# Performance work log

Hardware: AMD Instinct MI355X
Metric: run time of the kernel (lower is better)

## Reference

```python
import math
import jax, jax.numpy as jnp
import numpy as np

B, H, W, CV = 8, 64, 64, 256
T, CT = 77, 512
NH, TOP_M = 8, 5
CLAMP = 2.0

def _ln(x, g, b, eps=1e-5):
    mu = x.mean(-1, keepdims=True)
    var = ((x - mu) ** 2).mean(-1, keepdims=True)
    return (x - mu) / jnp.sqrt(var + eps) * g + b

def _l2norm(x, eps=1e-6):
    n = jnp.sqrt((x * x).sum(-1, keepdims=True))
    return x / jnp.maximum(n, eps)

def _xavier(key, fan_in, fan_out):
    a = math.sqrt(6.0 / (fan_in + fan_out))
    return jax.random.uniform(key, (fan_in, fan_out), jnp.float32, -a, a)

def setup_inputs() -> dict:
    key = jax.random.key(0)
    ks = jax.random.split(key, 12)
    inp = {
        'visual_features': jax.random.normal(ks[0], (B, H, W, CV), jnp.float32),
        'text_features': jax.random.normal(ks[1], (B, T, CT), jnp.float32),
        'Wq': _xavier(ks[2], CV, CV), 'bq': jnp.zeros((CV,), jnp.float32),
        'Wk': _xavier(ks[3], CT, CV), 'bk': jnp.zeros((CV,), jnp.float32),
        'Wv': _xavier(ks[4], CT, CV), 'bv': jnp.zeros((CV,), jnp.float32),
        'Wo': _xavier(ks[5], CV, CV), 'bo': jnp.zeros((CV,), jnp.float32),
        'g1': jnp.ones((CV,), jnp.float32), 'b1': jnp.zeros((CV,), jnp.float32),
        'g2': jnp.ones((CV,), jnp.float32), 'b2': jnp.zeros((CV,), jnp.float32),
        'W_ffn1': jax.random.normal(ks[6], (CV, 4 * CV), jnp.float32) * 0.02,
        'b_ffn1': jnp.zeros((4 * CV,), jnp.float32),
        'W_ffn2': jax.random.normal(ks[7], (4 * CV, CV), jnp.float32) * 0.02,
        'b_ffn2': jnp.zeros((CV,), jnp.float32),
        'logit_scale': jnp.float32(math.log(1.0 / 0.07)),
        'alpha': jnp.float32(0.1),
    }
    return inp

def _topm_mask(sim, m):
    # keep only top-m entries along last axis (scatter of top-k indices)
    t = sim.shape[-1]
    _, topi = jax.lax.top_k(sim, m)
    keep = jax.vmap(lambda idx: jnp.zeros((t,), bool).at[idx].set(True))(
        topi.reshape(-1, m)).reshape(sim.shape)
    return jnp.where(keep, sim, -jnp.inf)

def _forward(visual_features, text_features, Wq, bq, Wk, bk, Wv, bv, Wo, bo,
             g1, b1, g2, b2, W_ffn1, b_ffn1, W_ffn2, b_ffn2, logit_scale, alpha):
    b, h, w, cv = visual_features.shape
    n = h * w
    dh = cv // NH
    x = _ln(visual_features, g1, b1).reshape(b, n, cv)      # Pre-LN, (B,N,Cv)
    q = (x @ Wq + bq).reshape(b, n, NH, dh)
    k = (text_features @ Wk + bk).reshape(b, T, NH, dh)
    v = (text_features @ Wv + bv).reshape(b, T, NH, dh)
    q = _l2norm(q); k = _l2norm(k)                           # cosine attention
    scale = jnp.exp(jnp.clip(logit_scale, -CLAMP, CLAMP)) / jnp.sqrt(jnp.float32(dh))
    sim = jnp.einsum('bnhd,bthd->bnht', q, k) * scale        # (B,N,H,T)
    pad = jnp.abs(text_features).sum(-1) <= 1e-6             # (B,T) pad tokens
    sim = jnp.where(pad[:, None, None, :], -jnp.inf, sim)
    sim = _topm_mask(sim, TOP_M)
    attn = jax.nn.softmax(sim, axis=-1)
    all_pad = pad.all(axis=1)                                # (B,)
    attn = jnp.where(all_pad[:, None, None, None], 0.0, attn)
    aligned = jnp.einsum('bnht,bthd->bnhd', attn, v).reshape(b, n, cv)
    aligned = aligned @ Wo + bo
    y = x + alpha * aligned
    y = _ln(y, g2, b2)
    hdn = jax.nn.gelu(y @ W_ffn1 + b_ffn1, approximate=False)
    y = y + (hdn @ W_ffn2 + b_ffn2)
    return y.reshape(b, h, w, cv)

def reference(visual_features, text_features, Wq, bq, Wk, bk, Wv, bv, Wo, bo,
              g1, b1, g2, b2, W_ffn1, b_ffn1, W_ffn2, b_ffn2, logit_scale, alpha):
    return _forward(visual_features, text_features, Wq, bq, Wk, bk, Wv, bv, Wo, bo,
                    g1, b1, g2, b2, W_ffn1, b_ffn1, W_ffn2, b_ffn2, logit_scale, alpha)
```

## Files before the change

kernel.cpp:

```cpp
#include <hip/hip_runtime.h>
#include <math.h>

#define NB   8
#define NPIX 4096
#define MROW 32768
#define CV_  256
#define TT   77
#define CT_  512
#define NH_  8
#define DH_  32
#define BT_  616

typedef __bf16 bf16x8 __attribute__((ext_vector_type(8)));
typedef float  f32x4  __attribute__((ext_vector_type(4)));

__device__ __forceinline__ float bf2f(unsigned short u) {
  return __uint_as_float(((unsigned)u) << 16);
}
__device__ __forceinline__ unsigned short f2b(float f) {
  unsigned u = __float_as_uint(f);
  return (unsigned short)((u + 0x7FFFu + ((u >> 16) & 1u)) >> 16);
}
__device__ __forceinline__ unsigned pack2(float lo, float hi) {
  return ((unsigned)f2b(hi) << 16) | (unsigned)f2b(lo);
}
__device__ __forceinline__ void async_copy16(const unsigned short* g,
                                             unsigned short* l) {
  __builtin_amdgcn_global_load_lds(
      (const __attribute__((address_space(1))) void*)g,
      (__attribute__((address_space(3))) void*)l, 16, 0, 0);
}
__device__ __forceinline__ float gelu_t(float v) {
  float p = v * fmaf(0.0713548162726f, v * v, 1.59576912161f);
  float e = __expf(p);
  return v - v / (e + 1.0f);
}

__global__ __launch_bounds__(256) void prep_kernel(
    const float* __restrict__ visual, const float* __restrict__ g1,
    const float* __restrict__ b1, unsigned short* __restrict__ xbuf,
    const float* __restrict__ s0, const float* __restrict__ s1,
    const float* __restrict__ s2, const float* __restrict__ s3,
    const float* __restrict__ s4, const float* __restrict__ s5,
    unsigned short* __restrict__ d0, unsigned short* __restrict__ d1,
    unsigned short* __restrict__ d2, unsigned short* __restrict__ d3,
    unsigned short* __restrict__ d4, unsigned short* __restrict__ d5,
    const float* __restrict__ bk, const float* __restrict__ bv,
    float* __restrict__ bkv, const float* __restrict__ text,
    float* __restrict__ padb) {
  __shared__ unsigned short tl[64 * 68];
  int bx = blockIdx.x;
  int tid = threadIdx.x;
  int wave = tid >> 6, lane = tid & 63;
  if (bx < 8192) {
    int row = bx * 4 + wave;
    size_t base = (size_t)row * 256 + lane * 4;
    float4 f = *reinterpret_cast<const float4*>(visual + base);
    float v0 = f.x, v1 = f.y, v2 = f.z, v3 = f.w;
    float s = v0 + v1 + v2 + v3;
    float q = v0 * v0 + v1 * v1 + v2 * v2 + v3 * v3;
#pragma unroll
    for (int off = 1; off < 64; off <<= 1) {
      s += __shfl_xor(s, off);
      q += __shfl_xor(q, off);
    }
    float mean = s * (1.0f / 256.0f);
    float var  = q * (1.0f / 256.0f) - mean * mean;
    float rstd = rsqrtf(var + 1e-5f);
    float4 gv = *reinterpret_cast<const float4*>(g1 + lane * 4);
    float4 bv4 = *reinterpret_cast<const float4*>(b1 + lane * 4);
    ushort4 o;
    o.x = f2b((v0 - mean) * rstd * gv.x + bv4.x);
    o.y = f2b((v1 - mean) * rstd * gv.y + bv4.y);
    o.z = f2b((v2 - mean) * rstd * gv.z + bv4.z);
    o.w = f2b((v3 - mean) * rstd * gv.w + bv4.w);
    *reinterpret_cast<ushort4*>(xbuf + base) = o;
    return;
  }
  if (bx < 8416) {
    int ti = bx - 8192;
    const float* src; unsigned short* dst; int R, C, m;
    if      (ti < 16)  { src = s0; dst = d0; R = 256;  C = 256;  m = ti; }
    else if (ti < 48)  { src = s1; dst = d1; R = 512;  C = 256;  m = ti - 16; }
    else if (ti < 80)  { src = s2; dst = d2; R = 512;  C = 256;  m = ti - 48; }
    else if (ti < 96)  { src = s3; dst = d3; R = 256;  C = 256;  m = ti - 80; }
    else if (ti < 160) { src = s4; dst = d4; R = 256;  C = 1024; m = ti - 96; }
    else               { src = s5; dst = d5; R = 1024; C = 256;  m = ti - 160; }
    int tpc = C >> 6;
    int tr = m / tpc, tc = m % tpc;
#pragma unroll
    for (int i = 0; i < 4; ++i) {
      int lin = tid + i * 256;
      int r = lin >> 4, c4 = (lin & 15) * 4;
      float4 f = *reinterpret_cast<const float4*>(
          src + (size_t)(tr * 64 + r) * C + tc * 64 + c4);
      tl[(c4 + 0) * 68 + r] = f2b(f.x);
      tl[(c4 + 1) * 68 + r] = f2b(f.y);
      tl[(c4 + 2) * 68 + r] = f2b(f.z);
      tl[(c4 + 3) * 68 + r] = f2b(f.w);
    }
    __syncthreads();
#pragma unroll
    for (int i = 0; i < 4; ++i) {
      int lin = tid + i * 256;
      int c = lin >> 4, r4 = (lin & 15) * 4;
      ushort4 u = *reinterpret_cast<const ushort4*>(&tl[c * 68 + r4]);
      *reinterpret_cast<ushort4*>(
          dst + (size_t)(tc * 64 + c) * R + tr * 64 + r4) = u;
    }
    return;
  }
  if (bx == 8416) {
    bkv[tid] = bk[tid];
    bkv[256 + tid] = bv[tid];
    return;
  }
  {
    int row = (bx - 8417) * 4 + wave;
    const float* tr = text + (size_t)row * CT_ + lane * 8;
    float4 f0 = *reinterpret_cast<const float4*>(tr);
    float4 f1 = *reinterpret_cast<const float4*>(tr + 4);
    float s = fabsf(f0.x) + fabsf(f0.y) + fabsf(f0.z) + fabsf(f0.w)
            + fabsf(f1.x) + fabsf(f1.y) + fabsf(f1.z) + fabsf(f1.w);
#pragma unroll
    for (int off = 1; off < 64; off <<= 1) s += __shfl_xor(s, off);
    if (lane == 0) padb[row] = (s <= 1e-6f) ? 1.0f : 0.0f;
  }
}

__global__ __launch_bounds__(256) void qkv_kernel(
    const unsigned short* __restrict__ xb, const unsigned short* __restrict__ WqT,
    const float* __restrict__ bq, unsigned short* __restrict__ qout,
    const float* __restrict__ text, const unsigned short* __restrict__ WkvT,
    const float* __restrict__ bkv, float* __restrict__ kout,
    float* __restrict__ vout) {
  __shared__ unsigned short lA[4096];
  __shared__ unsigned short lB[4096];
  int tid = threadIdx.x;
  int lane = tid & 63, wave = tid >> 6;
  int l15 = lane & 15, quad = lane >> 4;
  if (blockIdx.x < 512) {
    int bm = (blockIdx.x >> 1) * 128, bn = (blockIdx.x & 1) * 128;
    int wm = (wave & 1) * 64, wn = (wave >> 1) * 64;
    int crow = lane >> 2, ccol = (lane & 3) * 8;
    f32x4 acc[4][4] = {};
    for (int k0 = 0; k0 < 256; k0 += 32) {
#pragma unroll
      for (int ch = 0; ch < 2; ++ch) {
        int c = wave * 2 + ch;
        async_copy16(xb + (size_t)(bm + c * 16 + crow) * 256 + k0 + ccol,
                     &lA[c * 512]);
        async_copy16(WqT + (size_t)(bn + c * 16 + crow) * 256 + k0 + ccol,
                     &lB[c * 512]);
      }
      __syncthreads();
      bf16x8 af[4], bfr[4];
#pragma unroll
      for (int mi = 0; mi < 4; ++mi)
        af[mi] = *reinterpret_cast<const bf16x8*>(&lA[(wm + mi * 16 + l15) * 32 + quad * 8]);
#pragma unroll
      for (int ni = 0; ni < 4; ++ni)
        bfr[ni] = *reinterpret_cast<const bf16x8*>(&lB[(wn + ni * 16 + l15) * 32 + quad * 8]);
#pragma unroll
      for (int mi = 0; mi < 4; ++mi)
#pragma unroll
        for (int ni = 0; ni < 4; ++ni)
          acc[mi][ni] = __builtin_amdgcn_mfma_f32_16x16x32_bf16(af[mi], bfr[ni],
                                                                acc[mi][ni], 0, 0, 0);
      __syncthreads();
    }
#pragma unroll
    for (int mi = 0; mi < 4; ++mi) {
#pragma unroll
      for (int ni = 0; ni < 4; ++ni) {
        int gcol = bn + wn + ni * 16 + l15;
        float bsf = bq[gcol];
#pragma unroll
        for (int r = 0; r < 4; ++r) {
          int grow = bm + wm + mi * 16 + quad * 4 + r;
          qout[(size_t)grow * 256 + gcol] = f2b(acc[mi][ni][r] + bsf);
        }
      }
    }
  } else {
    int i = blockIdx.x - 512;
    int bm = (i % 10) * 64, bn = (i / 10) * 64;
    int srow = tid >> 2, sc8 = (tid & 3) * 8;
    int wm = (wave & 1) * 32, wn = (wave >> 1) * 32;
    f32x4 acc[2][2] = {};
    int gm = bm + srow, gn = bn + srow;
    const bool aok = (gm < BT_);
    for (int k0 = 0; k0 < CT_; k0 += 32) {
      uint4 apk = make_uint4(0, 0, 0, 0);
      if (aok) {
        const float* Af = text + (size_t)gm * CT_ + k0 + sc8;
        float4 f0 = *reinterpret_cast<const float4*>(Af);
        float4 f1 = *reinterpret_cast<const float4*>(Af + 4);
        apk.x = pack2(f0.x, f0.y); apk.y = pack2(f0.z, f0.w);
        apk.z = pack2(f1.x, f1.y); apk.w = pack2(f1.z, f1.w);
      }
      uint4 bpk = *reinterpret_cast<const uint4*>(WkvT + (size_t)gn * CT_ + k0 + sc8);
      *reinterpret_cast<uint4*>(&lA[srow * 40 + sc8]) = apk;
      *reinterpret_cast<uint4*>(&lB[srow * 40 + sc8]) = bpk;
      __syncthreads();
      bf16x8 a0 = *reinterpret_cast<const bf16x8*>(&lA[(wm + l15) * 40 + quad * 8]);
      bf16x8 a1 = *reinterpret_cast<const bf16x8*>(&lA[(wm + 16 + l15) * 40 + quad * 8]);
      bf16x8 b0 = *reinterpret_cast<const bf16x8*>(&lB[(wn + l15) * 40 + quad * 8]);
      bf16x8 b1 = *reinterpret_cast<const bf16x8*>(&lB[(wn + 16 + l15) * 40 + quad * 8]);
      acc[0][0] = __builtin_amdgcn_mfma_f32_16x16x32_bf16(a0, b0, acc[0][0], 0, 0, 0);
      acc[0][1] = __builtin_amdgcn_mfma_f32_16x16x32_bf16(a0, b1, acc[0][1], 0, 0, 0);
      acc[1][0] = __builtin_amdgcn_mfma_f32_16x16x32_bf16(a1, b0, acc[1][0], 0, 0, 0);
      acc[1][1] = __builtin_amdgcn_mfma_f32_16x16x32_bf16(a1, b1, acc[1][1], 0, 0, 0);
      __syncthreads();
    }
#pragma unroll
    for (int mt = 0; mt < 2; ++mt) {
#pragma unroll
      for (int nt = 0; nt < 2; ++nt) {
        int gcol = bn + wn + nt * 16 + l15;
        float bsf = bkv[gcol];
#pragma unroll
        for (int r = 0; r < 4; ++r) {
          int grow = bm + wm + mt * 16 + quad * 4 + r;
          if (grow >= BT_) continue;
          float v = acc[mt][nt][r] + bsf;
          if (gcol < 256) kout[(size_t)grow * 256 + gcol] = v;
          else            vout[(size_t)grow * 256 + gcol - 256] = v;
        }
      }
    }
  }
}

__global__ __launch_bounds__(256) void gemm_oln(
    const unsigned short* __restrict__ A, const unsigned short* __restrict__ Bt,
    const float* __restrict__ bias, const unsigned short* __restrict__ xres,
    const float* __restrict__ alpha_ptr,
    const float* __restrict__ g2, const float* __restrict__ b2,
    unsigned short* __restrict__ ybf, float* __restrict__ yf32) {
  __shared__ unsigned short sm[16384];
  unsigned short* lA = sm;
  unsigned short* lB = sm + 2048;
  unsigned short* yt = sm;
  const int K = 256;
  int tid = threadIdx.x;
  int bm = blockIdx.x * 64;
  int lane = tid & 63, wave = tid >> 6;
  int wm = (wave & 1) * 32, wn = (wave >> 1) * 128;
  int l15 = lane & 15, quad = lane >> 4;
  int crow = lane >> 2, ccol = (lane & 3) * 8;
  f32x4 acc[2][8] = {};
  for (int k0 = 0; k0 < K; k0 += 32) {
    async_copy16(A + (size_t)(bm + wave * 16 + crow) * K + k0 + ccol,
                 &lA[wave * 512]);
#pragma unroll
    for (int ch = wave; ch < 16; ch += 4)
      async_copy16(Bt + (size_t)(ch * 16 + crow) * K + k0 + ccol,
                   &lB[ch * 512]);
    __syncthreads();
    bf16x8 af[2], bfr[8];
#pragma unroll
    for (int mi = 0; mi < 2; ++mi)
      af[mi] = *reinterpret_cast<const bf16x8*>(&lA[(wm + mi * 16 + l15) * 32 + quad * 8]);
#pragma unroll
    for (int ni = 0; ni < 8; ++ni)
      bfr[ni] = *reinterpret_cast<const bf16x8*>(&lB[(wn + ni * 16 + l15) * 32 + quad * 8]);
#pragma unroll
    for (int mi = 0; mi < 2; ++mi)
#pragma unroll
      for (int ni = 0; ni < 8; ++ni)
        acc[mi][ni] = __builtin_amdgcn_mfma_f32_16x16x32_bf16(af[mi], bfr[ni],
                                                              acc[mi][ni], 0, 0, 0);
    __syncthreads();
  }
  float alpha = *alpha_ptr;
#pragma unroll
  for (int mi = 0; mi < 2; ++mi) {
#pragma unroll
    for (int ni = 0; ni < 8; ++ni) {
      int gcol = wn + ni * 16 + l15;
      float bsf = bias[gcol];
#pragma unroll
      for (int r = 0; r < 4; ++r) {
        int lrow = wm + mi * 16 + quad * 4 + r;
        float v = acc[mi][ni][r] + bsf;
        float y0 = bf2f(xres[(size_t)(bm + lrow) * 256 + gcol]) + alpha * v;
        yt[lrow * 256 + gcol] = f2b(y0);
      }
    }
  }
  __syncthreads();
  for (int it = 0; it < 16; ++it) {
    int row = wave * 16 + it;
    ushort4 u = *reinterpret_cast<const ushort4*>(&yt[row * 256 + lane * 4]);
    float v0 = bf2f(u.x), v1 = bf2f(u.y), v2 = bf2f(u.z), v3 = bf2f(u.w);
    float s = v0 + v1 + v2 + v3;
    float q = v0 * v0 + v1 * v1 + v2 * v2 + v3 * v3;
#pragma unroll
    for (int off = 1; off < 64; off <<= 1) {
      s += __shfl_xor(s, off);
      q += __shfl_xor(q, off);
    }
    float mean = s * (1.0f / 256.0f);
    float var  = q * (1.0f / 256.0f) - mean * mean;
    float rstd = rsqrtf(var + 1e-5f);
    float4 gv = *reinterpret_cast<const float4*>(g2 + lane * 4);
    float4 bv = *reinterpret_cast<const float4*>(b2 + lane * 4);
    float o0 = (v0 - mean) * rstd * gv.x + bv.x;
    float o1 = (v1 - mean) * rstd * gv.y + bv.y;
    float o2 = (v2 - mean) * rstd * gv.z + bv.z;
    float o3 = (v3 - mean) * rstd * gv.w + bv.w;
    size_t base = (size_t)(bm + row) * 256 + lane * 4;
    ushort4 ob;
    ob.x = f2b(o0); ob.y = f2b(o1); ob.z = f2b(o2); ob.w = f2b(o3);
    *reinterpret_cast<ushort4*>(ybf + base) = ob;
    *reinterpret_cast<float4*>(yf32 + base) = make_float4(o0, o1, o2, o3);
  }
}

#define SSTR 83
#define VSTR 33
#define NEGBIG -3.0e38f
__device__ __forceinline__ void ins5(float sv, float& tv0, float& tv1,
                                     float& tv2, float& tv3, float& tv4) {
  bool g0 = sv > tv0, g1 = sv > tv1, g2 = sv > tv2, g3 = sv > tv3, g4 = sv > tv4;
  tv4 = g4 ? (g3 ? tv3 : sv) : tv4;
  tv3 = g3 ? (g2 ? tv2 : sv) : tv3;
  tv2 = g2 ? (g1 ? tv1 : sv) : tv2;
  tv1 = g1 ? (g0 ? tv0 : sv) : tv1;
  tv0 = g0 ? sv : tv0;
}
__global__ __launch_bounds__(256) void attn_kernel(
    unsigned short* qa, const float* __restrict__ k,
    const float* __restrict__ v, const float* __restrict__ padb,
    const float* __restrict__ ls_ptr) {
  __shared__ unsigned short qb[64 * 40];
  __shared__ unsigned short kb[80 * 40];
  __shared__ float S[64 * SSTR];
  __shared__ float vs[TT * VSTR];
  __shared__ float rn[64];
  __shared__ float scs[80];
  __shared__ int allpad_s;
  int tid = threadIdx.x;
  int h = blockIdx.y, b = blockIdx.z;
  size_t qbase = ((size_t)b * NPIX + blockIdx.x * 64) * CV_ + h * DH_;
  size_t kvbase = (size_t)b * TT * CV_ + h * DH_;
  float ls = *ls_ptr;
  ls = fminf(fmaxf(ls, -2.0f), 2.0f);
  float scale = expf(ls) * 0.17677669529663687f;
  if (tid == 0) allpad_s = 1;
  __syncthreads();
  int qrow = tid >> 2, qq = tid & 3;
  uint4 qv4 = *reinterpret_cast<const uint4*>(qa + qbase + (size_t)qrow * CV_ + qq * 8);
  *reinterpret_cast<uint4*>(&qb[qrow * 40 + qq * 8]) = qv4;
  {
    float ssq = 0.f;
    unsigned w[4] = {qv4.x, qv4.y, qv4.z, qv4.w};
#pragma unroll
    for (int i = 0; i < 4; ++i) {
      float a = bf2f((unsigned short)(w[i] & 0xFFFF));
      float bb = bf2f((unsigned short)(w[i] >> 16));
      ssq += a * a + bb * bb;
    }
    ssq += __shfl_xor(ssq, 1);
    ssq += __shfl_xor(ssq, 2);
    if (qq == 0) rn[qrow] = scale / fmaxf(sqrtf(ssq), 1e-6f);
  }
  if (tid < 154) {
    int kr = tid >> 1, kh = tid & 1;
    const float* kp = k + kvbase + (size_t)kr * CV_ + kh * 16;
    float4 f0 = *reinterpret_cast<const float4*>(kp);
    float4 f1 = *reinterpret_cast<const float4*>(kp + 4);
    float4 f2 = *reinterpret_cast<const float4*>(kp + 8);
    float4 f3 = *reinterpret_cast<const float4*>(kp + 12);
    float ks2 = f0.x*f0.x + f0.y*f0.y + f0.z*f0.z + f0.w*f0.w
              + f1.x*f1.x + f1.y*f1.y + f1.z*f1.z + f1.w*f1.w
              + f2.x*f2.x + f2.y*f2.y + f2.z*f2.z + f2.w*f2.w
              + f3.x*f3.x + f3.y*f3.y + f3.z*f3.z + f3.w*f3.w;
    uint4 p0, p1;
    p0.x = pack2(f0.x, f0.y); p0.y = pack2(f0.z, f0.w);
    p0.z = pack2(f1.x, f1.y); p0.w = pack2(f1.z, f1.w);
    p1.x = pack2(f2.x, f2.y); p1.y = pack2(f2.z, f2.w);
    p1.z = pack2(f3.x, f3.y); p1.w = pack2(f3.z, f3.w);
    *reinterpret_cast<uint4*>(&kb[kr * 40 + kh * 16]) = p0;
    *reinterpret_cast<uint4*>(&kb[kr * 40 + kh * 16 + 8]) = p1;
    ks2 += __shfl_xor(ks2, 1);
    if (kh == 0) {
      float p = padb[b * TT + kr];
      float sc = (p == 0.0f) ? 1.0f / fmaxf(sqrtf(ks2), 1e-6f) : 0.0f;
      scs[kr] = sc;
      if (sc > 0.0f) allpad_s = 0;
    }
  } else if (tid < 157) {
    scs[77 + (tid - 154)] = 0.0f;
  } else if (tid >= 160 && tid < 172) {
    int i = tid - 160;
    *reinterpret_cast<uint4*>(&kb[(77 + (i >> 2)) * 40 + (i & 3) * 8]) =
        make_uint4(0, 0, 0, 0);
  }
  for (int j = tid; j < TT * 8; j += 256) {
    int t = j >> 3, d4 = j & 7;
    float4 f = *reinterpret_cast<const float4*>(
        v + kvbase + (size_t)t * CV_ + d4 * 4);
    float* vp = &vs[t * VSTR + d4 * 4];
    vp[0] = f.x; vp[1] = f.y; vp[2] = f.z; vp[3] = f.w;
  }
  __syncthreads();
  {
    int lane = tid & 63, wave = tid >> 6;
    int wm = wave * 16;
    int l15 = lane & 15, quad = lane >> 4;
    f32x4 acc[5] = {};
    bf16x8 af = *reinterpret_cast<const bf16x8*>(&qb[(wm + l15) * 40 + quad * 8]);
    bf16x8 bfr[5];
#pragma unroll
    for (int ni = 0; ni < 5; ++ni)
      bfr[ni] = *reinterpret_cast<const bf16x8*>(&kb[(ni * 16 + l15) * 40 + quad * 8]);
#pragma unroll
    for (int ni = 0; ni < 5; ++ni)
      acc[ni] = __builtin_amdgcn_mfma_f32_16x16x32_bf16(af, bfr[ni], acc[ni], 0, 0, 0);
#pragma unroll
    for (int ni = 0; ni < 5; ++ni) {
      int col = ni * 16 + l15;
      float sc = scs[col];
#pragma unroll
      for (int r = 0; r < 4; ++r) {
        int row = wm + quad * 4 + r;
        float val = (sc > 0.0f) ? acc[ni][r] * rn[row] * sc : NEGBIG;
        unsigned pb = (__float_as_uint(val) & 0xFFFFFF80u) | (unsigned)col;
        S[row * SSTR + col] = __uint_as_float(pb);
      }
    }
  }
  __syncthreads();
  int allpad = allpad_s;
  int row = qrow;
  const float* Srow = &S[row * SSTR];
  int t0 = qq * 20, t1 = (qq == 3) ? TT : t0 + 20;
  float tv0 = -INFINITY, tv1 = -INFINITY, tv2 = -INFINITY,
        tv3 = -INFINITY, tv4 = -INFINITY;
  for (int t = t0; t < t1; ++t)
    ins5(Srow[t], tv0, tv1, tv2, tv3, tv4);
#pragma unroll
  for (int m = 1; m <= 2; m <<= 1) {
    float n0 = __shfl_xor(tv0, m), n1 = __shfl_xor(tv1, m),
          n2 = __shfl_xor(tv2, m), n3 = __shfl_xor(tv3, m),
          n4 = __shfl_xor(tv4, m);
    ins5(n0, tv0, tv1, tv2, tv3, tv4);
    ins5(n1, tv0, tv1, tv2, tv3, tv4);
    ins5(n2, tv0, tv1, tv2, tv3, tv4);
    ins5(n3, tv0, tv1, tv2, tv3, tv4);
    ins5(n4, tv0, tv1, tv2, tv3, tv4);
  }
  float o[8];
#pragma unroll
  for (int d = 0; d < 8; ++d) o[d] = 0.f;
  if (!allpad) {
    float e0 = 1.0f;
    float e1 = expf(tv1 - tv0);
    float e2 = expf(tv2 - tv0);
    float e3 = expf(tv3 - tv0);
    float e4 = expf(tv4 - tv0);
    float inv = 1.0f / (e0 + e1 + e2 + e3 + e4);
    int i0 = __float_as_uint(tv0) & 0x7F, i1 = __float_as_uint(tv1) & 0x7F,
        i2 = __float_as_uint(tv2) & 0x7F, i3 = __float_as_uint(tv3) & 0x7F,
        i4 = __float_as_uint(tv4) & 0x7F;
    const float* v0p = &vs[i0 * VSTR + qq * 8];
    const float* v1p = &vs[i1 * VSTR + qq * 8];
    const float* v2p = &vs[i2 * VSTR + qq * 8];
    const float* v3p = &vs[i3 * VSTR + qq * 8];
    const float* v4p = &vs[i4 * VSTR + qq * 8];
#pragma unroll
    for (int d = 0; d < 8; ++d)
      o[d] = (e0 * v0p[d] + e1 * v1p[d] + e2 * v2p[d] + e3 * v3p[d] + e4 * v4p[d]) * inv;
  }
  unsigned short* qp = qa + qbase + (size_t)row * CV_ + qq * 8;
  uint4 ou;
  ou.x = ((unsigned)f2b(o[1]) << 16) | f2b(o[0]);
  ou.y = ((unsigned)f2b(o[3]) << 16) | f2b(o[2]);
  ou.z = ((unsigned)f2b(o[5]) << 16) | f2b(o[4]);
  ou.w = ((unsigned)f2b(o[7]) << 16) | f2b(o[6]);
  *reinterpret_cast<uint4*>(qp) = ou;
}

#define XSTR 264
#define HSTR 136
__global__ __launch_bounds__(512) void ffn_fused(
    const unsigned short* __restrict__ ybf, const unsigned short* __restrict__ W1T,
    const float* __restrict__ b1f, const unsigned short* __restrict__ W2T,
    const float* __restrict__ b2f, float* __restrict__ yio) {
  __shared__ unsigned short xs[128 * XSTR];
  __shared__ unsigned short Hs[128 * HSTR];
  __shared__ unsigned short Wb[16384];
  int tid = threadIdx.x, lane = tid & 63, wave = tid >> 6;
  int l15 = lane & 15, quad = lane >> 4;
  int crow = lane >> 2;
  int ccs = (((lane & 3) ^ ((lane >> 3) & 3)) * 8);
  int rsw = ((quad ^ ((l15 >> 1) & 3)) * 8);
  int bm = blockIdx.x * 128;
  {
    int row = tid >> 2, kh = (tid & 3) * 64;
    const unsigned short* src = ybf + (size_t)(bm + row) * 256 + kh;
    unsigned short* dst = &xs[row * XSTR + kh];
#pragma unroll
    for (int i = 0; i < 8; ++i)
      *reinterpret_cast<uint4*>(dst + i * 8) =
          *reinterpret_cast<const uint4*>(src + i * 8);
  }
  int wm2 = (wave & 1) * 64, wn2 = (wave >> 1) * 64;
  int wh1 = (wave & 1) * 64, wr1 = (wave >> 1) * 32;
  const unsigned short* w1p = W1T + (size_t)(wave * 16 + crow) * 256 + ccs;
  const unsigned short* w2p = W2T + (size_t)(wave * 32 + crow) * 1024 + ccs;
  auto stage_step = [&](int p2, int half) {
    unsigned short* buf = &Wb[half * 8192];
    if (p2 < 4) {
      async_copy16(w1p,      &buf[wave * 512]);
      async_copy16(w1p + 32, &buf[4096 + wave * 512]);
      w1p += 64;
      if (p2 == 3) w1p += 32512;
    } else {
      async_copy16(w2p,          &buf[wave * 1024]);
      async_copy16(w2p + 16384,  &buf[wave * 1024 + 512]);
      w2p += 32;
    }
  };
  f32x4 acc[4][4] = {};
  stage_step(0, 0); stage_step(1, 1);
  for (int c = 0; c < 8; ++c) {
    f32x4 acc1[4][2] = {};
#pragma unroll
    for (int p = 0; p < 8; ++p) {
      if (p == 7 && c == 7)
        asm volatile("s_waitcnt vmcnt(0) lgkmcnt(0)" ::: "memory");
      else
        asm volatile("s_waitcnt vmcnt(2) lgkmcnt(0)" ::: "memory");
      __builtin_amdgcn_s_barrier();
      __builtin_amdgcn_sched_barrier(0);
      const unsigned short* buf = &Wb[(p & 1) * 8192];
      if (p < 4) {
#pragma unroll
        for (int sl = 0; sl < 2; ++sl) {
          int k = p * 64 + sl * 32;
          bf16x8 af[4], bfr[2];
#pragma unroll
          for (int mi = 0; mi < 4; ++mi)
            af[mi] = *reinterpret_cast<const bf16x8*>(
                &buf[sl * 4096 + (wh1 + mi * 16 + l15) * 32 + rsw]);
#pragma unroll
          for (int ni = 0; ni < 2; ++ni)
            bfr[ni] = *reinterpret_cast<const bf16x8*>(
                &xs[(wr1 + ni * 16 + l15) * XSTR + k + quad * 8]);
          __builtin_amdgcn_s_setprio(1);
#pragma unroll
          for (int mi = 0; mi < 4; ++mi)
#pragma unroll
            for (int ni = 0; ni < 2; ++ni)
              acc1[mi][ni] = __builtin_amdgcn_mfma_f32_16x16x32_bf16(
                  af[mi], bfr[ni], acc1[mi][ni], 0, 0, 0);
          __builtin_amdgcn_s_setprio(0);
        }
        if (p == 3) {
#pragma unroll
          for (int mi = 0; mi < 4; ++mi) {
            int hb = wh1 + mi * 16 + quad * 4;
            float b0 = b1f[c * 128 + hb],      b1v = b1f[c * 128 + hb + 1];
            float b2v = b1f[c * 128 + hb + 2], b3 = b1f[c * 128 + hb + 3];
#pragma unroll
            for (int ni = 0; ni < 2; ++ni) {
              int row = wr1 + ni * 16 + l15;
              ushort4 hw;
              hw.x = f2b(gelu_t(acc1[mi][ni][0] + b0));
              hw.y = f2b(gelu_t(acc1[mi][ni][1] + b1v));
              hw.z = f2b(gelu_t(acc1[mi][ni][2] + b2v));
              hw.w = f2b(gelu_t(acc1[mi][ni][3] + b3));
              *reinterpret_cast<ushort4*>(&Hs[row * HSTR + hb]) = hw;
            }
          }
        }
      } else {
        int kk = (p - 4) * 32;
        bf16x8 af[4], bfr[4];
#pragma unroll
        for (int mi = 0; mi < 4; ++mi)
          af[mi] = *reinterpret_cast<const bf16x8*>(
              &Hs[(wm2 + mi * 16 + l15) * HSTR + kk + quad * 8]);
#pragma unroll
        for (int ni = 0; ni < 4; ++ni)
          bfr[ni] = *reinterpret_cast<const bf16x8*>(
              &buf[(wn2 + ni * 16 + l15) * 32 + rsw]);
        __builtin_amdgcn_s_setprio(1);
#pragma unroll
        for (int mi = 0; mi < 4; ++mi)
#pragma unroll
          for (int ni = 0; ni < 4; ++ni)
            acc[mi][ni] = __builtin_amdgcn_mfma_f32_16x16x32_bf16(
                af[mi], bfr[ni], acc[mi][ni], 0, 0, 0);
        __builtin_amdgcn_s_setprio(0);
      }
      __builtin_amdgcn_sched_barrier(0);
      __builtin_amdgcn_s_barrier();
      __builtin_amdgcn_sched_barrier(0);
      if (c < 7 || p < 6)
        stage_step((p + 2) & 7, p & 1);
    }
  }
#pragma unroll
  for (int mi = 0; mi < 4; ++mi)
#pragma unroll
    for (int ni = 0; ni < 4; ++ni) {
      int col = wn2 + ni * 16 + l15;
      float bs = b2f[col];
#pragma unroll
      for (int r = 0; r < 4; ++r) {
        int g = bm + wm2 + mi * 16 + quad * 4 + r;
        size_t oi = (size_t)g * 256 + col;
        yio[oi] = yio[oi] + acc[mi][ni][r] + bs;
      }
    }
}

extern "C" void kernel_launch(void* const* d_in, const int* in_sizes, int n_in,
                              void* d_out, int out_size, void* d_ws, size_t ws_size,
                              hipStream_t stream) {
  const float* visual = (const float*)d_in[0];
  const float* text   = (const float*)d_in[1];
  const float* Wq  = (const float*)d_in[2];
  const float* bq  = (const float*)d_in[3];
  const float* Wk  = (const float*)d_in[4];
  const float* bk  = (const float*)d_in[5];
  const float* Wv  = (const float*)d_in[6];
  const float* bv  = (const float*)d_in[7];
  const float* Wo  = (const float*)d_in[8];
  const float* bo  = (const float*)d_in[9];
  const float* g1  = (const float*)d_in[10];
  const float* b1  = (const float*)d_in[11];
  const float* g2  = (const float*)d_in[12];
  const float* b2  = (const float*)d_in[13];
  const float* W1  = (const float*)d_in[14];
  const float* bf1 = (const float*)d_in[15];
  const float* W2  = (const float*)d_in[16];
  const float* bff2 = (const float*)d_in[17];
  const float* lsc = (const float*)d_in[18];
  const float* alp = (const float*)d_in[19];

  char* ws = (char*)d_ws;
  size_t off = 0;
  auto alloc = [&](size_t bytes) -> char* {
    char* p = ws + off;
    off += (bytes + 255) & ~(size_t)255;
    return p;
  };
  unsigned short* WqT = (unsigned short*)alloc((size_t)65536 * 2);
  unsigned short* WkT = (unsigned short*)alloc((size_t)131072 * 2);
  unsigned short* WvT = (unsigned short*)alloc((size_t)131072 * 2);
  unsigned short* WoT = (unsigned short*)alloc((size_t)65536 * 2);
  unsigned short* W1T = (unsigned short*)alloc((size_t)262144 * 2);
  unsigned short* W2T = (unsigned short*)alloc((size_t)262144 * 2);
  float*          bkv  = (float*)alloc(512 * 4);
  float*          kbuf = (float*)alloc((size_t)BT_ * CV_ * 4);
  float*          vbuf = (float*)alloc((size_t)BT_ * CV_ * 4);
  float*          padb = (float*)alloc((size_t)BT_ * 4);
  char* U = ws + off;
  unsigned short* xbuf = (unsigned short*)U;
  unsigned short* qbuf = (unsigned short*)(U + 16777216);
  float*          ybuf = (float*)d_out;

  prep_kernel<<<8571, 256, 0, stream>>>(visual, g1, b1, xbuf,
                                        Wq, Wk, Wv, Wo, W1, W2,
                                        WqT, WkT, WvT, WoT, W1T, W2T,
                                        bk, bv, bkv, text, padb);
  qkv_kernel<<<592, 256, 0, stream>>>(xbuf, WqT, bq, qbuf,
                                      text, WkT, bkv, kbuf, vbuf);
  attn_kernel<<<dim3(64, NH_, NB), 256, 0, stream>>>(qbuf, kbuf, vbuf, padb, lsc);
  gemm_oln<<<512, 256, 0, stream>>>(qbuf, WoT, bo, xbuf, alp, g2, b2,
                                    xbuf, ybuf);
  ffn_fused<<<256, 512, 0, stream>>>(xbuf, W1T, bf1, W2T, bff2, ybuf);
}
```

Before: 285.5 us.

## Halve FFN row tile to 64 and XOR-swizzle shared-memory activations

```diff
diff --git a/kernel.cpp b/kernel.cpp
--- a/kernel.cpp
+++ b/kernel.cpp
@@ -483,32 +483,33 @@
   *reinterpret_cast<uint4*>(qp) = ou;
 }
 
-#define XSTR 264
-#define HSTR 136
 __global__ __launch_bounds__(512) void ffn_fused(
     const unsigned short* __restrict__ ybf, const unsigned short* __restrict__ W1T,
     const float* __restrict__ b1f, const unsigned short* __restrict__ W2T,
     const float* __restrict__ b2f, float* __restrict__ yio) {
-  __shared__ unsigned short xs[128 * XSTR];
-  __shared__ unsigned short Hs[128 * HSTR];
+  __shared__ unsigned short xs[64 * 256];
+  __shared__ unsigned short Hs[64 * 128];
   __shared__ unsigned short Wb[16384];
   int tid = threadIdx.x, lane = tid & 63, wave = tid >> 6;
   int l15 = lane & 15, quad = lane >> 4;
   int crow = lane >> 2;
   int ccs = (((lane & 3) ^ ((lane >> 3) & 3)) * 8);
   int rsw = ((quad ^ ((l15 >> 1) & 3)) * 8);
-  int bm = blockIdx.x * 128;
+  int sws = (l15 >> 1) & 3;
+  int bm = blockIdx.x * 64;
   {
-    int row = tid >> 2, kh = (tid & 3) * 64;
-    const unsigned short* src = ybf + (size_t)(bm + row) * 256 + kh;
-    unsigned short* dst = &xs[row * XSTR + kh];
-#pragma unroll
-    for (int i = 0; i < 8; ++i)
-      *reinterpret_cast<uint4*>(dst + i * 8) =
+    int row = tid >> 3, kh8 = (tid & 7) * 4;
+    const unsigned short* src = ybf + (size_t)(bm + row) * 256 + kh8 * 8;
+    int sw = (row >> 1) & 3;
+    unsigned short* dst = &xs[row * 256];
+#pragma unroll
+    for (int i = 0; i < 4; ++i)
+      *reinterpret_cast<uint4*>(dst + ((kh8 + i) ^ sw) * 8) =
           *reinterpret_cast<const uint4*>(src + i * 8);
   }
-  int wm2 = (wave & 1) * 64, wn2 = (wave >> 1) * 64;
-  int wh1 = (wave & 1) * 64, wr1 = (wave >> 1) * 32;
+  int wm2 = (wave & 1) * 32, wn2 = (wave >> 1) * 64;
+  int wh1 = (wave & 1) * 64, wr1 = (wave >> 1) * 16;
+  int row1 = wr1 + l15;
   const unsigned short* w1p = W1T + (size_t)(wave * 16 + crow) * 256 + ccs;
   const unsigned short* w2p = W2T + (size_t)(wave * 32 + crow) * 1024 + ccs;
   auto stage_step = [&](int p2, int half) {
@@ -524,10 +525,10 @@
       w2p += 32;
     }
   };
-  f32x4 acc[4][4] = {};
+  f32x4 acc[2][4] = {};
   stage_step(0, 0); stage_step(1, 1);
   for (int c = 0; c < 8; ++c) {
-    f32x4 acc1[4][2] = {};
+    f32x4 acc1[4] = {};
 #pragma unroll
     for (int p = 0; p < 8; ++p) {
       if (p == 7 && c == 7)
@@ -541,22 +542,18 @@
 #pragma unroll
         for (int sl = 0; sl < 2; ++sl) {
           int k = p * 64 + sl * 32;
-          bf16x8 af[4], bfr[2];
+          bf16x8 af[4];
 #pragma unroll
           for (int mi = 0; mi < 4; ++mi)
             af[mi] = *reinterpret_cast<const bf16x8*>(
                 &buf[sl * 4096 + (wh1 + mi * 16 + l15) * 32 + rsw]);
-#pragma unroll
-          for (int ni = 0; ni < 2; ++ni)
-            bfr[ni] = *reinterpret_cast<const bf16x8*>(
-                &xs[(wr1 + ni * 16 + l15) * XSTR + k + quad * 8]);
+          bf16x8 bx = *reinterpret_cast<const bf16x8*>(
+              &xs[row1 * 256 + (((k >> 3) + quad) ^ sws) * 8]);
           __builtin_amdgcn_s_setprio(1);
 #pragma unroll
           for (int mi = 0; mi < 4; ++mi)
-#pragma unroll
-            for (int ni = 0; ni < 2; ++ni)
-              acc1[mi][ni] = __builtin_amdgcn_mfma_f32_16x16x32_bf16(
-                  af[mi], bfr[ni], acc1[mi][ni], 0, 0, 0);
+            acc1[mi] = __builtin_amdgcn_mfma_f32_16x16x32_bf16(
+                af[mi], bx, acc1[mi], 0, 0, 0);
           __builtin_amdgcn_s_setprio(0);
         }
         if (p == 3) {
@@ -565,32 +562,31 @@
             int hb = wh1 + mi * 16 + quad * 4;
             float b0 = b1f[c * 128 + hb],      b1v = b1f[c * 128 + hb + 1];
             float b2v = b1f[c * 128 + hb + 2], b3 = b1f[c * 128 + hb + 3];
-#pragma unroll
-            for (int ni = 0; ni < 2; ++ni) {
-              int row = wr1 + ni * 16 + l15;
-              ushort4 hw;
-              hw.x = f2b(gelu_t(acc1[mi][ni][0] + b0));
-              hw.y = f2b(gelu_t(acc1[mi][ni][1] + b1v));
-              hw.z = f2b(gelu_t(acc1[mi][ni][2] + b2v));
-              hw.w = f2b(gelu_t(acc1[mi][ni][3] + b3));
-              *reinterpret_cast<ushort4*>(&Hs[row * HSTR + hb]) = hw;
-            }
+            ushort4 hw;
+            hw.x = f2b(gelu_t(acc1[mi][0] + b0));
+            hw.y = f2b(gelu_t(acc1[mi][1] + b1v));
+            hw.z = f2b(gelu_t(acc1[mi][2] + b2v));
+            hw.w = f2b(gelu_t(acc1[mi][3] + b3));
+            *reinterpret_cast<ushort4*>(
+                &Hs[row1 * 128 + (((hb >> 3) ^ sws) * 8) + (hb & 7)]) = hw;
           }
         }
       } else {
         int kk = (p - 4) * 32;
-        bf16x8 af[4], bfr[4];
-#pragma unroll
-        for (int mi = 0; mi < 4; ++mi)
+        bf16x8 af[2], bfr[4];
+#pragma unroll
+        for (int mi = 0; mi < 2; ++mi) {
+          int hrow = wm2 + mi * 16 + l15;
           af[mi] = *reinterpret_cast<const bf16x8*>(
-              &Hs[(wm2 + mi * 16 + l15) * HSTR + kk + quad * 8]);
+              &Hs[hrow * 128 + (((kk >> 3) + quad) ^ sws) * 8]);
+        }
 #pragma unroll
         for (int ni = 0; ni < 4; ++ni)
           bfr[ni] = *reinterpret_cast<const bf16x8*>(
               &buf[(wn2 + ni * 16 + l15) * 32 + rsw]);
         __builtin_amdgcn_s_setprio(1);
 #pragma unroll
-        for (int mi = 0; mi < 4; ++mi)
+        for (int mi = 0; mi < 2; ++mi)
 #pragma unroll
           for (int ni = 0; ni < 4; ++ni)
             acc[mi][ni] = __builtin_amdgcn_mfma_f32_16x16x32_bf16(
@@ -605,7 +601,7 @@
     }
   }
 #pragma unroll
-  for (int mi = 0; mi < 4; ++mi)
+  for (int mi = 0; mi < 2; ++mi)
 #pragma unroll
     for (int ni = 0; ni < 4; ++ni) {
       int col = wn2 + ni * 16 + l15;
@@ -674,5 +670,5 @@
   attn_kernel<<<dim3(64, NH_, NB), 256, 0, stream>>>(qbuf, kbuf, vbuf, padb, lsc);
   gemm_oln<<<512, 256, 0, stream>>>(qbuf, WoT, bo, xbuf, alp, g2, b2,
                                     xbuf, ybuf);
-  ffn_fused<<<256, 512, 0, stream>>>(xbuf, W1T, bf1, W2T, bff2, ybuf);
-}
+  ffn_fused<<<512, 512, 0, stream>>>(xbuf, W1T, bf1, W2T, bff2, ybuf);
+}
```

New measurement: 280.4 us. No clear change (-1.8%).
